# Optimization experiments

Hardware: AMD Instinct MI355X
Metric: run time of the kernel (lower is better)

## Reference

```python
import jax, jax.numpy as jnp
import numpy as np

NUM_HEADS = 12


def _build_mask(N, unseen_size, dtype):
    # Columns for the last `unseen_size` tokens are masked (-inf) for every
    # query row EXCEPT the diagonal entries in that block (each unseen token
    # may attend to itself). Matches the original Python-loop construction.
    idx = jnp.arange(N)
    col_unseen = idx[None, :] >= (N - unseen_size)
    off_diag = idx[:, None] != idx[None, :]
    return jnp.where(col_unseen & off_diag, -jnp.inf, jnp.asarray(0.0, dtype))


def reference(x, w_qkv, w_proj, b_proj, unseen_size):
    B, N, C = x.shape
    H = NUM_HEADS
    d = C // H
    scale = d ** -0.5
    # qkv: (B,N,3C) -> (3,B,H,N,d)
    qkv = (x @ w_qkv.T).reshape(B, N, 3, H, d).transpose(2, 0, 3, 1, 4)
    q, k, v = qkv[0], qkv[1], qkv[2]
    attn = jnp.einsum('bhqd,bhkd->bhqk', q, k) * scale
    attn = attn + _build_mask(N, unseen_size, attn.dtype)  # broadcast (N,N)
    attn = jax.nn.softmax(attn, axis=-1)
    out = jnp.einsum('bhqk,bhkd->bhqd', attn, v)
    out = out.transpose(0, 2, 1, 3).reshape(B, N, C)
    return out @ w_proj.T + b_proj


def setup_inputs() -> dict:
    key = jax.random.key(0)
    k1, k2, k3 = jax.random.split(key, 3)
    B, N, C = 2, 2048, 768
    x = jax.random.normal(k1, (B, N, C), dtype=jnp.float32)
    w_qkv = jax.random.normal(k2, (3 * C, C), dtype=jnp.float32) * (C ** -0.5)
    w_proj = jax.random.normal(k3, (C, C), dtype=jnp.float32) * (C ** -0.5)
    b_proj = jnp.zeros((C,), dtype=jnp.float32)
    return {"x": x, "w_qkv": w_qkv, "w_proj": w_proj, "b_proj": b_proj,
            "unseen_size": 512}
```

## Files before the change

kernel.cpp:

```cpp
#include <hip/hip_runtime.h>
#include <math.h>

#define NH 12
#define DH 64
#define NSEQ 2048
#define NB 2
#define CDIM 768
#define NVIS 1536

typedef _Float16 half8 __attribute__((ext_vector_type(8)));
typedef _Float16 half4 __attribute__((ext_vector_type(4)));
typedef float floatx4 __attribute__((ext_vector_type(4)));

static constexpr size_t SZ_X    = (size_t)NB*NSEQ*CDIM;
static constexpr size_t SZ_WQKV = (size_t)3*CDIM*CDIM;
static constexpr size_t SZ_WP   = (size_t)CDIM*CDIM;
static constexpr size_t SZ_HEAD = (size_t)NB*NH*NSEQ*DH;

#define GLOAD_LDS16(gp, lp) \
  __builtin_amdgcn_global_load_lds((const __attribute__((address_space(1))) void*)(gp), \
                                   (__attribute__((address_space(3))) void*)(lp), 16, 0, 0)

__global__ __launch_bounds__(256) void convert_kernel(
    const float* __restrict__ x, const float* __restrict__ wqkv, const float* __restrict__ wp,
    _Float16* __restrict__ xb, _Float16* __restrict__ wqkvb, _Float16* __restrict__ wpb)
{
  size_t idx = ((size_t)blockIdx.x*256 + threadIdx.x)*4;
  const float* src; _Float16* dst; size_t off;
  if (idx < SZ_X)                        { src = x;    dst = xb;    off = idx; }
  else if (idx < SZ_X+SZ_WQKV)           { src = wqkv; dst = wqkvb; off = idx - SZ_X; }
  else if (idx < SZ_X+SZ_WQKV+SZ_WP)     { src = wp;   dst = wpb;   off = idx - SZ_X - SZ_WQKV; }
  else return;
  float4 v = *reinterpret_cast<const float4*>(src + off);
  _Float16 o[4] = {(_Float16)v.x,(_Float16)v.y,(_Float16)v.z,(_Float16)v.w};
  *reinterpret_cast<uint2*>(dst + off) = *reinterpret_cast<uint2*>(o);
}

template<int MODE, int BN>
__global__ __launch_bounds__(256) void gemm_bt(
    const _Float16* __restrict__ A, const _Float16* __restrict__ Bt,
    const float* __restrict__ bias,
    _Float16* __restrict__ qb, _Float16* __restrict__ kb, _Float16* __restrict__ vb,
    float* __restrict__ outp)
{
  constexpr int K = CDIM;
  constexpr int BM = 128, BK = 32;
  constexpr int MI = (BN == 128) ? 4 : 2;
  constexpr int NI = 4;
  __shared__ _Float16 As[BM*BK];
  __shared__ _Float16 Bs[BN*BK];
  const int tid = threadIdx.x;
  const int lane = tid & 63, wid = tid >> 6;
  const int l15 = lane & 15, quad = lane >> 4;
  const int wm = (BN == 128) ? (wid >> 1)*64 : wid*32;
  const int wn = (BN == 128) ? (wid & 1)*64 : 0;
  const int tileN = blockIdx.x*BN, tileM = blockIdx.y*BM;
  const int lrow = lane >> 2, lchunk = lane & 3;
  const int gcol = ((lchunk ^ (lrow >> 1)) & 3)*8;
  const _Float16* gA0 = A  + (size_t)(tileM + wid*32      + lrow)*K + gcol;
  const _Float16* gA1 = A  + (size_t)(tileM + wid*32 + 16 + lrow)*K + gcol;
  const _Float16* gB0 = Bt + (size_t)(tileN + ((BN==128) ? wid*32 : wid*16) + lrow)*K + gcol;
  const _Float16* gB1 = Bt + (size_t)(tileN + wid*32 + 16 + lrow)*K + gcol;
  _Float16* lA0 = As + (wid*32)*BK;
  _Float16* lA1 = As + (wid*32 + 16)*BK;
  _Float16* lB0 = Bs + ((BN==128) ? wid*32 : wid*16)*BK;
  _Float16* lB1 = Bs + (wid*32 + 16)*BK;
  const int cp = ((quad ^ (l15 >> 1)) & 3)*8;
  floatx4 acc[MI][NI] = {};
  for (int k0 = 0; k0 < K; k0 += BK) {
    __syncthreads();
    GLOAD_LDS16(gA0 + k0, lA0);
    GLOAD_LDS16(gA1 + k0, lA1);
    GLOAD_LDS16(gB0 + k0, lB0);
    if (BN == 128) GLOAD_LDS16(gB1 + k0, lB1);
    __syncthreads();
    half8 af[MI], bfr[NI];
    #pragma unroll
    for (int mi = 0; mi < MI; mi++)
      af[mi] = *reinterpret_cast<const half8*>(&As[(wm + mi*16 + l15)*BK + cp]);
    #pragma unroll
    for (int ni = 0; ni < NI; ni++)
      bfr[ni] = *reinterpret_cast<const half8*>(&Bs[(wn + ni*16 + l15)*BK + cp]);
    #pragma unroll
    for (int mi = 0; mi < MI; mi++)
      #pragma unroll
      for (int ni = 0; ni < NI; ni++)
        acc[mi][ni] = __builtin_amdgcn_mfma_f32_16x16x32_f16(af[mi], bfr[ni], acc[mi][ni], 0,0,0);
  }
  #pragma unroll
  for (int mi = 0; mi < MI; mi++)
    #pragma unroll
    for (int ni = 0; ni < NI; ni++) {
      int n = tileN + wn + ni*16 + l15;
      int m0 = tileM + wm + mi*16 + quad*4;
      if (MODE == 0) {
        int part = n / CDIM, rem = n - part*CDIM;
        int h = rem >> 6, dd = rem & 63;
        int b = m0 >> 11, i0 = m0 & 2047;
        if (part == 2) {
          half4 pk = {(_Float16)acc[mi][ni][0], (_Float16)acc[mi][ni][1],
                      (_Float16)acc[mi][ni][2], (_Float16)acc[mi][ni][3]};
          *reinterpret_cast<half4*>(&vb[(((size_t)b*NH + h)*DH + dd)*NSEQ + i0]) = pk;
        } else {
          _Float16* dst = part ? kb : qb;
          float sc = part ? 1.0f : 0.125f*1.44269504f;
          #pragma unroll
          for (int r = 0; r < 4; r++)
            dst[(((size_t)b*NH + h)*NSEQ + i0 + r)*DH + dd] = (_Float16)(acc[mi][ni][r]*sc);
        }
      } else {
        #pragma unroll
        for (int r = 0; r < 4; r++)
          outp[(size_t)(m0 + r)*CDIM + n] = acc[mi][ni][r] + bias[n];
      }
    }
}

__global__ __launch_bounds__(256, 3) void fa_kernel(
    const _Float16* __restrict__ qg, const _Float16* __restrict__ kg,
    const _Float16* __restrict__ vtg, _Float16* __restrict__ og)
{
  constexpr int LDP = 136;
  __shared__ _Float16 Ps[64*LDP];
  __shared__ float Ls[4*64];
  const int blk = blockIdx.x;
  const int idx = blk >> 3;
  const int bh = (blk & 7)*3 + (idx % 3);
  const int qbase = (idx / 3) * 64;
  const int tid = threadIdx.x;
  const int lane = tid & 63, w = tid >> 6;
  const int l15 = lane & 15, quad = lane >> 4;
  const _Float16* qp  = qg  + (size_t)bh*NSEQ*DH;
  const _Float16* kbp = kg  + (size_t)bh*NSEQ*DH;
  const _Float16* vbp = vtg + (size_t)bh*DH*NSEQ;
  half8 qf[4][2];
  #pragma unroll
  for (int g = 0; g < 4; g++)
    #pragma unroll
    for (int c = 0; c < 2; c++)
      qf[g][c] = *reinterpret_cast<const half8*>(qp + (size_t)(qbase + g*16 + l15)*DH + c*32 + quad*8);
  const _Float16* kRow = kbp + (size_t)(w*16 + l15)*DH + quad*8;
  const _Float16* vRow = vbp + (size_t)(w*16 + l15)*NSEQ + quad*8;
  half8 kc[2][2], vc[2][2];
  #pragma unroll
  for (int s = 0; s < 2; s++)
    #pragma unroll
    for (int c = 0; c < 2; c++) {
      kc[s][c] = *reinterpret_cast<const half8*>(kRow + (size_t)(s*64)*DH + c*32);
      vc[s][c] = *reinterpret_cast<const half8*>(vRow + s*64 + c*32);
    }
  floatx4 o[4] = {};
  float lsum[4] = {0.f, 0.f, 0.f, 0.f};
  for (int t = 0; t < 12; t++) {
    const int tn = (t + 1 < 12) ? t + 1 : 0;
    half8 kn[2][2], vn[2][2];
    #pragma unroll
    for (int s = 0; s < 2; s++)
      #pragma unroll
      for (int c = 0; c < 2; c++) {
        kn[s][c] = *reinterpret_cast<const half8*>(kRow + (size_t)(tn*128 + s*64)*DH + c*32);
        vn[s][c] = *reinterpret_cast<const half8*>(vRow + tn*128 + s*64 + c*32);
      }
    half4 pk[2][4];
    #pragma unroll
    for (int s = 0; s < 2; s++) {
      floatx4 st[4] = {};
      #pragma unroll
      for (int g = 0; g < 4; g++) {
        st[g] = __builtin_amdgcn_mfma_f32_16x16x32_f16(kc[s][0], qf[g][0], st[g], 0,0,0);
        st[g] = __builtin_amdgcn_mfma_f32_16x16x32_f16(kc[s][1], qf[g][1], st[g], 0,0,0);
      }
      #pragma unroll
      for (int g = 0; g < 4; g++) {
        float e0 = __builtin_exp2f(st[g][0]), e1 = __builtin_exp2f(st[g][1]);
        float e2 = __builtin_exp2f(st[g][2]), e3 = __builtin_exp2f(st[g][3]);
        lsum[g] += (e0+e1)+(e2+e3);
        pk[s][g] = half4{(_Float16)e0,(_Float16)e1,(_Float16)e2,(_Float16)e3};
      }
    }
    __syncthreads();
    #pragma unroll
    for (int s = 0; s < 2; s++)
      #pragma unroll
      for (int g = 0; g < 4; g++)
        *reinterpret_cast<half4*>(&Ps[(g*16+l15)*LDP + s*64 + w*16 + quad*4]) = pk[s][g];
    __syncthreads();
    #pragma unroll
    for (int g = 0; g < 4; g++) {
      #pragma unroll
      for (int s = 0; s < 2; s++)
        #pragma unroll
        for (int c = 0; c < 2; c++) {
          half8 pb = *reinterpret_cast<const half8*>(&Ps[(g*16+l15)*LDP + s*64 + c*32 + quad*8]);
          o[g] = __builtin_amdgcn_mfma_f32_16x16x32_f16(vc[s][c], pb, o[g], 0,0,0);
        }
    }
    #pragma unroll
    for (int s = 0; s < 2; s++)
      #pragma unroll
      for (int c = 0; c < 2; c++) { kc[s][c] = kn[s][c]; vc[s][c] = vn[s][c]; }
  }
  #pragma unroll
  for (int g = 0; g < 4; g++) {
    lsum[g] += __shfl_xor(lsum[g], 16);
    lsum[g] += __shfl_xor(lsum[g], 32);
  }
  if (lane < 16) {
    #pragma unroll
    for (int g = 0; g < 4; g++) Ls[w*64 + g*16 + lane] = lsum[g];
  }
  __syncthreads();
  float den[4];
  #pragma unroll
  for (int g = 0; g < 4; g++)
    den[g] = Ls[g*16+l15] + Ls[64+g*16+l15] + Ls[128+g*16+l15] + Ls[192+g*16+l15];
  if (qbase >= NVIS) {
    #pragma unroll
    for (int g = 0; g < 4; g++) {
      half8 kd0 = *reinterpret_cast<const half8*>(kbp + (size_t)(qbase + g*16 + l15)*DH + quad*8);
      half8 kd1 = *reinterpret_cast<const half8*>(kbp + (size_t)(qbase + g*16 + l15)*DH + 32 + quad*8);
      float pd = 0.f;
      #pragma unroll
      for (int j = 0; j < 8; j++)
        pd += (float)qf[g][0][j]*(float)kd0[j] + (float)qf[g][1][j]*(float)kd1[j];
      pd += __shfl_xor(pd, 16);
      pd += __shfl_xor(pd, 32);
      float e = __builtin_exp2f(pd);
      den[g] += e;
      #pragma unroll
      for (int r = 0; r < 4; r++)
        o[g][r] += e * (float)vbp[(size_t)(w*16+quad*4+r)*NSEQ + qbase + g*16 + l15];
    }
  }
  const int b = bh / NH, h = bh - b*NH;
  #pragma unroll
  for (int g = 0; g < 4; g++) {
    float inv = 1.0f / den[g];
    half4 pk = {(_Float16)(o[g][0]*inv), (_Float16)(o[g][1]*inv),
                (_Float16)(o[g][2]*inv), (_Float16)(o[g][3]*inv)};
    size_t oaddr = ((size_t)b*NSEQ + qbase + g*16 + l15)*CDIM + h*DH + w*16 + quad*4;
    *reinterpret_cast<half4*>(&og[oaddr]) = pk;
  }
}

extern "C" void kernel_launch(void* const* d_in, const int* in_sizes, int n_in,
                              void* d_out, int out_size, void* d_ws, size_t ws_size,
                              hipStream_t stream) {
  (void)in_sizes; (void)n_in; (void)out_size; (void)ws_size;
  const float* x     = (const float*)d_in[0];
  const float* wqkv  = (const float*)d_in[1];
  const float* wproj = (const float*)d_in[2];
  const float* bproj = (const float*)d_in[3];

  _Float16* xb    = (_Float16*)d_ws;
  _Float16* wqkvb = xb + SZ_X;
  _Float16* wpb   = wqkvb + SZ_WQKV;
  _Float16* qb    = wpb + SZ_WP;
  _Float16* kb    = qb + SZ_HEAD;
  _Float16* vb    = kb + SZ_HEAD;
  _Float16* ob    = vb + SZ_HEAD;
  float* outp = (float*)d_out;

  size_t total = SZ_X + SZ_WQKV + SZ_WP;
  int cblocks = (int)((total/4 + 255)/256);
  convert_kernel<<<cblocks, 256, 0, stream>>>(x, wqkv, wproj, xb, wqkvb, wpb);
  gemm_bt<0,128><<<dim3(3*CDIM/128, NB*NSEQ/128), 256, 0, stream>>>(xb, wqkvb, nullptr, qb, kb, vb, nullptr);
  fa_kernel<<<NB*NH*(NSEQ/64), 256, 0, stream>>>(qb, kb, vb, ob);
  gemm_bt<1,64><<<dim3(CDIM/64, NB*NSEQ/128), 256, 0, stream>>>(ob, wpb, bproj, nullptr, nullptr, nullptr, outp);
}
```

Before: 166.0 us.

## Restructure attention kernel: LDS double-buffered K/V, register-shuffled P, 2 waves

The attention kernel moves from 4 waves that each load their own K/V slices from global into registers and exchange P through LDS with two barriers per step, to 2 waves that each own 32 query rows. K and V tiles of 64 keys are now staged into swizzled, double-buffered LDS with async global-to-LDS loads. P is repacked in registers with cross-lane shuffles and packed fp16 conversion instead of going through shared memory. The aim is to remove the P round-trip through LDS and the duplicated K/V fetches, at the cost of more shuffles, fewer waves per block, and a lower occupancy hint.

```diff
diff --git a/kernel.cpp b/kernel.cpp
--- a/kernel.cpp
+++ b/kernel.cpp
@@ -10,6 +10,7 @@
 
 typedef _Float16 half8 __attribute__((ext_vector_type(8)));
 typedef _Float16 half4 __attribute__((ext_vector_type(4)));
+typedef __fp16 fp16x2 __attribute__((ext_vector_type(2)));
 typedef float floatx4 __attribute__((ext_vector_type(4)));
 
 static constexpr size_t SZ_X    = (size_t)NB*NSEQ*CDIM;
@@ -20,6 +21,12 @@
 #define GLOAD_LDS16(gp, lp) \
   __builtin_amdgcn_global_load_lds((const __attribute__((address_space(1))) void*)(gp), \
                                    (__attribute__((address_space(3))) void*)(lp), 16, 0, 0)
+
+static __device__ __forceinline__ int pack_e2(float a, float b) {
+  union { fp16x2 h; int i; } u;
+  u.h = __builtin_amdgcn_cvt_pkrtz(a, b);
+  return u.i;
+}
 
 __global__ __launch_bounds__(256) void convert_kernel(
     const float* __restrict__ x, const float* __restrict__ wqkv, const float* __restrict__ wp,
@@ -116,13 +123,12 @@
     }
 }
 
-__global__ __launch_bounds__(256, 3) void fa_kernel(
+__global__ __launch_bounds__(128, 2) void fa_kernel(
     const _Float16* __restrict__ qg, const _Float16* __restrict__ kg,
     const _Float16* __restrict__ vtg, _Float16* __restrict__ og)
 {
-  constexpr int LDP = 136;
-  __shared__ _Float16 Ps[64*LDP];
-  __shared__ float Ls[4*64];
+  __shared__ _Float16 Ks[2][64*64];
+  __shared__ _Float16 Vs[2][64*64];
   const int blk = blockIdx.x;
   const int idx = blk >> 3;
   const int bh = (blk & 7)*3 + (idx % 3);
@@ -133,92 +139,95 @@
   const _Float16* qp  = qg  + (size_t)bh*NSEQ*DH;
   const _Float16* kbp = kg  + (size_t)bh*NSEQ*DH;
   const _Float16* vbp = vtg + (size_t)bh*DH*NSEQ;
-  half8 qf[4][2];
-  #pragma unroll
-  for (int g = 0; g < 4; g++)
+  half8 qf[2][2];
+  #pragma unroll
+  for (int g = 0; g < 2; g++)
     #pragma unroll
     for (int c = 0; c < 2; c++)
-      qf[g][c] = *reinterpret_cast<const half8*>(qp + (size_t)(qbase + g*16 + l15)*DH + c*32 + quad*8);
-  const _Float16* kRow = kbp + (size_t)(w*16 + l15)*DH + quad*8;
-  const _Float16* vRow = vbp + (size_t)(w*16 + l15)*NSEQ + quad*8;
-  half8 kc[2][2], vc[2][2];
-  #pragma unroll
-  for (int s = 0; s < 2; s++)
-    #pragma unroll
-    for (int c = 0; c < 2; c++) {
-      kc[s][c] = *reinterpret_cast<const half8*>(kRow + (size_t)(s*64)*DH + c*32);
-      vc[s][c] = *reinterpret_cast<const half8*>(vRow + s*64 + c*32);
-    }
-  floatx4 o[4] = {};
-  float lsum[4] = {0.f, 0.f, 0.f, 0.f};
-  for (int t = 0; t < 12; t++) {
-    const int tn = (t + 1 < 12) ? t + 1 : 0;
-    half8 kn[2][2], vn[2][2];
-    #pragma unroll
-    for (int s = 0; s < 2; s++)
+      qf[g][c] = *reinterpret_cast<const half8*>(
+          qp + (size_t)(qbase + w*32 + g*16 + l15)*DH + c*32 + quad*8);
+  const int strow = w*32 + (lane >> 3);
+  const int sgch  = ((lane & 7) ^ (lane >> 3)) * 8;
+  const int rdoff0 = l15*64 + (((0*4 + quad) ^ (l15 & 7))*8);
+  const int rdoff1 = l15*64 + (((1*4 + quad) ^ (l15 & 7))*8);
+  const int bidx0 = ((quad & 1)*2)*16 + l15;
+  const int bidx1 = bidx0 + 16;
+  const bool hiq = (quad >> 1) != 0;
+
+  floatx4 o[2][4] = {};
+  float lsum[2] = {0.f, 0.f};
+
+  #pragma unroll
+  for (int u = 0; u < 4; u++) {
+    GLOAD_LDS16(kbp + (size_t)(strow + u*8)*DH + sgch,        &Ks[0][(w*32 + u*8)*64]);
+    GLOAD_LDS16(vbp + (size_t)(strow + u*8)*NSEQ + 0 + sgch,  &Vs[0][(w*32 + u*8)*64]);
+  }
+  for (int t = 0; t < 24; t++) {
+    const int buf = t & 1;
+    __syncthreads();
+    if (t < 23) {
+      const int kvn = (t + 1)*64;
+      #pragma unroll
+      for (int u = 0; u < 4; u++) {
+        GLOAD_LDS16(kbp + (size_t)(kvn + strow + u*8)*DH + sgch,   &Ks[buf^1][(w*32 + u*8)*64]);
+        GLOAD_LDS16(vbp + (size_t)(strow + u*8)*NSEQ + kvn + sgch, &Vs[buf^1][(w*32 + u*8)*64]);
+      }
+    }
+    half8 kf[4][2], vf[4][2];
+    #pragma unroll
+    for (int f = 0; f < 4; f++) {
+      kf[f][0] = *reinterpret_cast<const half8*>(&Ks[buf][f*1024 + rdoff0]);
+      kf[f][1] = *reinterpret_cast<const half8*>(&Ks[buf][f*1024 + rdoff1]);
+      vf[f][0] = *reinterpret_cast<const half8*>(&Vs[buf][f*1024 + rdoff0]);
+      vf[f][1] = *reinterpret_cast<const half8*>(&Vs[buf][f*1024 + rdoff1]);
+    }
+    int srcdw[2][4][2];
+    #pragma unroll
+    for (int g = 0; g < 2; g++)
+      #pragma unroll
+      for (int f = 0; f < 4; f++) {
+        floatx4 st = {};
+        st = __builtin_amdgcn_mfma_f32_16x16x32_f16(kf[f][0], qf[g][0], st, 0,0,0);
+        st = __builtin_amdgcn_mfma_f32_16x16x32_f16(kf[f][1], qf[g][1], st, 0,0,0);
+        float e0 = __builtin_exp2f(st[0]), e1 = __builtin_exp2f(st[1]);
+        float e2 = __builtin_exp2f(st[2]), e3 = __builtin_exp2f(st[3]);
+        lsum[g] += (e0 + e1) + (e2 + e3);
+        srcdw[g][f][0] = pack_e2(e0, e1);
+        srcdw[g][f][1] = pack_e2(e2, e3);
+      }
+    #pragma unroll
+    for (int g = 0; g < 2; g++) {
       #pragma unroll
       for (int c = 0; c < 2; c++) {
-        kn[s][c] = *reinterpret_cast<const half8*>(kRow + (size_t)(tn*128 + s*64)*DH + c*32);
-        vn[s][c] = *reinterpret_cast<const half8*>(vRow + tn*128 + s*64 + c*32);
-      }
-    half4 pk[2][4];
-    #pragma unroll
-    for (int s = 0; s < 2; s++) {
-      floatx4 st[4] = {};
-      #pragma unroll
-      for (int g = 0; g < 4; g++) {
-        st[g] = __builtin_amdgcn_mfma_f32_16x16x32_f16(kc[s][0], qf[g][0], st[g], 0,0,0);
-        st[g] = __builtin_amdgcn_mfma_f32_16x16x32_f16(kc[s][1], qf[g][1], st[g], 0,0,0);
-      }
-      #pragma unroll
-      for (int g = 0; g < 4; g++) {
-        float e0 = __builtin_exp2f(st[g][0]), e1 = __builtin_exp2f(st[g][1]);
-        float e2 = __builtin_exp2f(st[g][2]), e3 = __builtin_exp2f(st[g][3]);
-        lsum[g] += (e0+e1)+(e2+e3);
-        pk[s][g] = half4{(_Float16)e0,(_Float16)e1,(_Float16)e2,(_Float16)e3};
-      }
-    }
-    __syncthreads();
-    #pragma unroll
-    for (int s = 0; s < 2; s++)
-      #pragma unroll
-      for (int g = 0; g < 4; g++)
-        *reinterpret_cast<half4*>(&Ps[(g*16+l15)*LDP + s*64 + w*16 + quad*4]) = pk[s][g];
-    __syncthreads();
-    #pragma unroll
-    for (int g = 0; g < 4; g++) {
-      #pragma unroll
-      for (int s = 0; s < 2; s++)
+        union { int i[4]; half8 v; } pbu;
         #pragma unroll
-        for (int c = 0; c < 2; c++) {
-          half8 pb = *reinterpret_cast<const half8*>(&Ps[(g*16+l15)*LDP + s*64 + c*32 + quad*8]);
-          o[g] = __builtin_amdgcn_mfma_f32_16x16x32_f16(vc[s][c], pb, o[g], 0,0,0);
+        for (int p = 0; p < 4; p++) {
+          const int ix = (p >> 1) ? bidx1 : bidx0;
+          int tA = __shfl(srcdw[g][2*c][p & 1], ix);
+          int tB = __shfl(srcdw[g][2*c + 1][p & 1], ix);
+          pbu.i[p] = hiq ? tB : tA;
         }
-    }
-    #pragma unroll
-    for (int s = 0; s < 2; s++)
-      #pragma unroll
-      for (int c = 0; c < 2; c++) { kc[s][c] = kn[s][c]; vc[s][c] = vn[s][c]; }
-  }
-  #pragma unroll
-  for (int g = 0; g < 4; g++) {
-    lsum[g] += __shfl_xor(lsum[g], 16);
-    lsum[g] += __shfl_xor(lsum[g], 32);
-  }
-  if (lane < 16) {
-    #pragma unroll
-    for (int g = 0; g < 4; g++) Ls[w*64 + g*16 + lane] = lsum[g];
-  }
-  __syncthreads();
-  float den[4];
-  #pragma unroll
-  for (int g = 0; g < 4; g++)
-    den[g] = Ls[g*16+l15] + Ls[64+g*16+l15] + Ls[128+g*16+l15] + Ls[192+g*16+l15];
+        o[g][0] = __builtin_amdgcn_mfma_f32_16x16x32_f16(vf[0][c], pbu.v, o[g][0], 0,0,0);
+        o[g][1] = __builtin_amdgcn_mfma_f32_16x16x32_f16(vf[1][c], pbu.v, o[g][1], 0,0,0);
+        o[g][2] = __builtin_amdgcn_mfma_f32_16x16x32_f16(vf[2][c], pbu.v, o[g][2], 0,0,0);
+        o[g][3] = __builtin_amdgcn_mfma_f32_16x16x32_f16(vf[3][c], pbu.v, o[g][3], 0,0,0);
+      }
+    }
+  }
+  float den[2];
+  #pragma unroll
+  for (int g = 0; g < 2; g++) {
+    float s = lsum[g];
+    s += __shfl_xor(s, 16);
+    s += __shfl_xor(s, 32);
+    den[g] = s;
+  }
   if (qbase >= NVIS) {
     #pragma unroll
-    for (int g = 0; g < 4; g++) {
-      half8 kd0 = *reinterpret_cast<const half8*>(kbp + (size_t)(qbase + g*16 + l15)*DH + quad*8);
-      half8 kd1 = *reinterpret_cast<const half8*>(kbp + (size_t)(qbase + g*16 + l15)*DH + 32 + quad*8);
+    for (int g = 0; g < 2; g++) {
+      const int q_abs = qbase + w*32 + g*16 + l15;
+      half8 kd0 = *reinterpret_cast<const half8*>(kbp + (size_t)q_abs*DH + quad*8);
+      half8 kd1 = *reinterpret_cast<const half8*>(kbp + (size_t)q_abs*DH + 32 + quad*8);
       float pd = 0.f;
       #pragma unroll
       for (int j = 0; j < 8; j++)
@@ -228,18 +237,24 @@
       float e = __builtin_exp2f(pd);
       den[g] += e;
       #pragma unroll
-      for (int r = 0; r < 4; r++)
-        o[g][r] += e * (float)vbp[(size_t)(w*16+quad*4+r)*NSEQ + qbase + g*16 + l15];
+      for (int df = 0; df < 4; df++)
+        #pragma unroll
+        for (int r = 0; r < 4; r++)
+          o[g][df][r] += e * (float)vbp[(size_t)(df*16 + quad*4 + r)*NSEQ + q_abs];
     }
   }
   const int b = bh / NH, h = bh - b*NH;
   #pragma unroll
-  for (int g = 0; g < 4; g++) {
-    float inv = 1.0f / den[g];
-    half4 pk = {(_Float16)(o[g][0]*inv), (_Float16)(o[g][1]*inv),
-                (_Float16)(o[g][2]*inv), (_Float16)(o[g][3]*inv)};
-    size_t oaddr = ((size_t)b*NSEQ + qbase + g*16 + l15)*CDIM + h*DH + w*16 + quad*4;
-    *reinterpret_cast<half4*>(&og[oaddr]) = pk;
+  for (int g = 0; g < 2; g++) {
+    const float inv = 1.0f / den[g];
+    const int q_abs = qbase + w*32 + g*16 + l15;
+    size_t obase = ((size_t)b*NSEQ + q_abs)*CDIM + h*DH + quad*4;
+    #pragma unroll
+    for (int df = 0; df < 4; df++) {
+      half4 pk = {(_Float16)(o[g][df][0]*inv), (_Float16)(o[g][df][1]*inv),
+                  (_Float16)(o[g][df][2]*inv), (_Float16)(o[g][df][3]*inv)};
+      *reinterpret_cast<half4*>(&og[obase + df*16]) = pk;
+    }
   }
 }
 
@@ -265,6 +280,6 @@
   int cblocks = (int)((total/4 + 255)/256);
   convert_kernel<<<cblocks, 256, 0, stream>>>(x, wqkv, wproj, xb, wqkvb, wpb);
   gemm_bt<0,128><<<dim3(3*CDIM/128, NB*NSEQ/128), 256, 0, stream>>>(xb, wqkvb, nullptr, qb, kb, vb, nullptr);
-  fa_kernel<<<NB*NH*(NSEQ/64), 256, 0, stream>>>(qb, kb, vb, ob);
+  fa_kernel<<<NB*NH*(NSEQ/64), 128, 0, stream>>>(qb, kb, vb, ob);
   gemm_bt<1,64><<<dim3(CDIM/64, NB*NSEQ/128), 256, 0, stream>>>(ob, wpb, bproj, nullptr, nullptr, nullptr, outp);
 }
```

Measured after the change: 175.5 us. 1.06x slower.

## Split attention KV range across two blocks and add combine kernel

Applied to the files above, without the earlier changes.

The attention kernel now splits the 1536 visible keys into two halves handled by separate blocks, doubling the grid and halving the per-iteration tile. It writes unnormalized fp32 partial outputs and denominators to workspace. A new combine kernel sums the partials, adds the diagonal unseen term and normalizes. The aim is better occupancy and more parallelism (768 to 1536 blocks, launch bounds 6). The cost is an extra launch and fp32 partial traffic through global memory.

```diff
diff --git a/kernel.cpp b/kernel.cpp
--- a/kernel.cpp
+++ b/kernel.cpp
@@ -16,6 +16,8 @@
 static constexpr size_t SZ_WQKV = (size_t)3*CDIM*CDIM;
 static constexpr size_t SZ_WP   = (size_t)CDIM*CDIM;
 static constexpr size_t SZ_HEAD = (size_t)NB*NH*NSEQ*DH;
+static constexpr size_t SZ_OPART = (size_t)2*24*32*64*64;
+static constexpr size_t SZ_DEN   = (size_t)2*24*32*64;
 
 #define GLOAD_LDS16(gp, lp) \
   __builtin_amdgcn_global_load_lds((const __attribute__((address_space(1))) void*)(gp), \
@@ -116,17 +118,22 @@
     }
 }
 
-__global__ __launch_bounds__(256, 3) void fa_kernel(
+__global__ __launch_bounds__(256, 6) void fa_kernel(
     const _Float16* __restrict__ qg, const _Float16* __restrict__ kg,
-    const _Float16* __restrict__ vtg, _Float16* __restrict__ og)
+    const _Float16* __restrict__ vtg, float* __restrict__ opart,
+    float* __restrict__ denp)
 {
-  constexpr int LDP = 136;
+  constexpr int LDP = 72;
   __shared__ _Float16 Ps[64*LDP];
   __shared__ float Ls[4*64];
   const int blk = blockIdx.x;
   const int idx = blk >> 3;
   const int bh = (blk & 7)*3 + (idx % 3);
-  const int qbase = (idx / 3) * 64;
+  const int rest = idx / 3;
+  const int qtile = rest >> 1;
+  const int sb = rest & 1;
+  const int qbase = qtile * 64;
+  const int kvoff = sb * 768;
   const int tid = threadIdx.x;
   const int lane = tid & 63, w = tid >> 6;
   const int l15 = lane & 15, quad = lane >> 4;
@@ -139,66 +146,47 @@
     #pragma unroll
     for (int c = 0; c < 2; c++)
       qf[g][c] = *reinterpret_cast<const half8*>(qp + (size_t)(qbase + g*16 + l15)*DH + c*32 + quad*8);
-  const _Float16* kRow = kbp + (size_t)(w*16 + l15)*DH + quad*8;
-  const _Float16* vRow = vbp + (size_t)(w*16 + l15)*NSEQ + quad*8;
-  half8 kc[2][2], vc[2][2];
-  #pragma unroll
-  for (int s = 0; s < 2; s++)
-    #pragma unroll
-    for (int c = 0; c < 2; c++) {
-      kc[s][c] = *reinterpret_cast<const half8*>(kRow + (size_t)(s*64)*DH + c*32);
-      vc[s][c] = *reinterpret_cast<const half8*>(vRow + s*64 + c*32);
-    }
+  const _Float16* kRow = kbp + (size_t)(kvoff + w*16 + l15)*DH + quad*8;
+  const _Float16* vRow = vbp + (size_t)(w*16 + l15)*NSEQ + kvoff + quad*8;
+  half8 kc0 = *reinterpret_cast<const half8*>(kRow);
+  half8 kc1 = *reinterpret_cast<const half8*>(kRow + 32);
+  half8 vc0 = *reinterpret_cast<const half8*>(vRow);
+  half8 vc1 = *reinterpret_cast<const half8*>(vRow + 32);
   floatx4 o[4] = {};
   float lsum[4] = {0.f, 0.f, 0.f, 0.f};
   for (int t = 0; t < 12; t++) {
     const int tn = (t + 1 < 12) ? t + 1 : 0;
-    half8 kn[2][2], vn[2][2];
-    #pragma unroll
-    for (int s = 0; s < 2; s++)
-      #pragma unroll
-      for (int c = 0; c < 2; c++) {
-        kn[s][c] = *reinterpret_cast<const half8*>(kRow + (size_t)(tn*128 + s*64)*DH + c*32);
-        vn[s][c] = *reinterpret_cast<const half8*>(vRow + tn*128 + s*64 + c*32);
-      }
-    half4 pk[2][4];
-    #pragma unroll
-    for (int s = 0; s < 2; s++) {
-      floatx4 st[4] = {};
-      #pragma unroll
-      for (int g = 0; g < 4; g++) {
-        st[g] = __builtin_amdgcn_mfma_f32_16x16x32_f16(kc[s][0], qf[g][0], st[g], 0,0,0);
-        st[g] = __builtin_amdgcn_mfma_f32_16x16x32_f16(kc[s][1], qf[g][1], st[g], 0,0,0);
-      }
-      #pragma unroll
-      for (int g = 0; g < 4; g++) {
-        float e0 = __builtin_exp2f(st[g][0]), e1 = __builtin_exp2f(st[g][1]);
-        float e2 = __builtin_exp2f(st[g][2]), e3 = __builtin_exp2f(st[g][3]);
-        lsum[g] += (e0+e1)+(e2+e3);
-        pk[s][g] = half4{(_Float16)e0,(_Float16)e1,(_Float16)e2,(_Float16)e3};
-      }
+    half8 kn0 = *reinterpret_cast<const half8*>(kRow + (size_t)tn*64*DH);
+    half8 kn1 = *reinterpret_cast<const half8*>(kRow + (size_t)tn*64*DH + 32);
+    half8 vn0 = *reinterpret_cast<const half8*>(vRow + tn*64);
+    half8 vn1 = *reinterpret_cast<const half8*>(vRow + tn*64 + 32);
+    floatx4 st[4] = {};
+    #pragma unroll
+    for (int g = 0; g < 4; g++) {
+      st[g] = __builtin_amdgcn_mfma_f32_16x16x32_f16(kc0, qf[g][0], st[g], 0,0,0);
+      st[g] = __builtin_amdgcn_mfma_f32_16x16x32_f16(kc1, qf[g][1], st[g], 0,0,0);
+    }
+    half4 pk[4];
+    #pragma unroll
+    for (int g = 0; g < 4; g++) {
+      float e0 = __builtin_exp2f(st[g][0]), e1 = __builtin_exp2f(st[g][1]);
+      float e2 = __builtin_exp2f(st[g][2]), e3 = __builtin_exp2f(st[g][3]);
+      lsum[g] += (e0+e1)+(e2+e3);
+      pk[g] = half4{(_Float16)e0,(_Float16)e1,(_Float16)e2,(_Float16)e3};
     }
     __syncthreads();
     #pragma unroll
-    for (int s = 0; s < 2; s++)
-      #pragma unroll
-      for (int g = 0; g < 4; g++)
-        *reinterpret_cast<half4*>(&Ps[(g*16+l15)*LDP + s*64 + w*16 + quad*4]) = pk[s][g];
+    for (int g = 0; g < 4; g++)
+      *reinterpret_cast<half4*>(&Ps[(g*16+l15)*LDP + w*16 + quad*4]) = pk[g];
     __syncthreads();
     #pragma unroll
     for (int g = 0; g < 4; g++) {
-      #pragma unroll
-      for (int s = 0; s < 2; s++)
-        #pragma unroll
-        for (int c = 0; c < 2; c++) {
-          half8 pb = *reinterpret_cast<const half8*>(&Ps[(g*16+l15)*LDP + s*64 + c*32 + quad*8]);
-          o[g] = __builtin_amdgcn_mfma_f32_16x16x32_f16(vc[s][c], pb, o[g], 0,0,0);
-        }
+      half8 pb0 = *reinterpret_cast<const half8*>(&Ps[(g*16+l15)*LDP + quad*8]);
+      half8 pb1 = *reinterpret_cast<const half8*>(&Ps[(g*16+l15)*LDP + 32 + quad*8]);
+      o[g] = __builtin_amdgcn_mfma_f32_16x16x32_f16(vc0, pb0, o[g], 0,0,0);
+      o[g] = __builtin_amdgcn_mfma_f32_16x16x32_f16(vc1, pb1, o[g], 0,0,0);
     }
-    #pragma unroll
-    for (int s = 0; s < 2; s++)
-      #pragma unroll
-      for (int c = 0; c < 2; c++) { kc[s][c] = kn[s][c]; vc[s][c] = vn[s][c]; }
+    kc0 = kn0; kc1 = kn1; vc0 = vn0; vc1 = vn1;
   }
   #pragma unroll
   for (int g = 0; g < 4; g++) {
@@ -210,37 +198,78 @@
     for (int g = 0; g < 4; g++) Ls[w*64 + g*16 + lane] = lsum[g];
   }
   __syncthreads();
-  float den[4];
+  float* op = opart + (((size_t)sb*24 + bh)*32 + qtile)*4096;
   #pragma unroll
   for (int g = 0; g < 4; g++)
-    den[g] = Ls[g*16+l15] + Ls[64+g*16+l15] + Ls[128+g*16+l15] + Ls[192+g*16+l15];
+    #pragma unroll
+    for (int r = 0; r < 4; r++)
+      op[(w*16 + quad*4 + r)*64 + g*16 + l15] = o[g][r];
+  if (w == 0) {
+    float dsum = Ls[lane] + Ls[64+lane] + Ls[128+lane] + Ls[192+lane];
+    denp[(((size_t)sb*24 + bh)*32 + qtile)*64 + lane] = dsum;
+  }
+}
+
+__global__ __launch_bounds__(256) void combine_kernel(
+    const float* __restrict__ opart, const float* __restrict__ denp,
+    const _Float16* __restrict__ qg, const _Float16* __restrict__ kg,
+    const _Float16* __restrict__ vtg, _Float16* __restrict__ og)
+{
+  __shared__ float Ot[64*65];
+  __shared__ float Dn[64];
+  const int bh = blockIdx.x >> 5;
+  const int qtile = blockIdx.x & 31;
+  const int qbase = qtile * 64;
+  const int t = threadIdx.x;
+  const float* opA = opart + ((size_t)bh*32 + qtile)*4096;
+  const float* opB = opart + ((size_t)(24 + bh)*32 + qtile)*4096;
+  if (t < 64)
+    Dn[t] = denp[((size_t)bh*32 + qtile)*64 + t]
+          + denp[((size_t)(24 + bh)*32 + qtile)*64 + t];
+  #pragma unroll
+  for (int i = 0; i < 16; i++) {
+    int idx = i*256 + t;
+    int d = idx >> 6, q = idx & 63;
+    Ot[d*65 + q] = opA[idx] + opB[idx];
+  }
+  __syncthreads();
+  const int q = t >> 2, ds = (t & 3)*16;
+  const int q_abs = qbase + q;
+  float ov[16];
+  #pragma unroll
+  for (int j = 0; j < 16; j++) ov[j] = Ot[(ds + j)*65 + q];
+  float den = Dn[q];
   if (qbase >= NVIS) {
-    #pragma unroll
-    for (int g = 0; g < 4; g++) {
-      half8 kd0 = *reinterpret_cast<const half8*>(kbp + (size_t)(qbase + g*16 + l15)*DH + quad*8);
-      half8 kd1 = *reinterpret_cast<const half8*>(kbp + (size_t)(qbase + g*16 + l15)*DH + 32 + quad*8);
-      float pd = 0.f;
-      #pragma unroll
-      for (int j = 0; j < 8; j++)
-        pd += (float)qf[g][0][j]*(float)kd0[j] + (float)qf[g][1][j]*(float)kd1[j];
-      pd += __shfl_xor(pd, 16);
-      pd += __shfl_xor(pd, 32);
-      float e = __builtin_exp2f(pd);
-      den[g] += e;
-      #pragma unroll
-      for (int r = 0; r < 4; r++)
-        o[g][r] += e * (float)vbp[(size_t)(w*16+quad*4+r)*NSEQ + qbase + g*16 + l15];
-    }
-  }
+    const _Float16* qrow = qg + ((size_t)bh*NSEQ + q_abs)*DH + ds;
+    const _Float16* krow = kg + ((size_t)bh*NSEQ + q_abs)*DH + ds;
+    half8 qa = *reinterpret_cast<const half8*>(qrow);
+    half8 qb2 = *reinterpret_cast<const half8*>(qrow + 8);
+    half8 ka = *reinterpret_cast<const half8*>(krow);
+    half8 kb2 = *reinterpret_cast<const half8*>(krow + 8);
+    float pd = 0.f;
+    #pragma unroll
+    for (int j = 0; j < 8; j++)
+      pd += (float)qa[j]*(float)ka[j] + (float)qb2[j]*(float)kb2[j];
+    pd += __shfl_xor(pd, 1);
+    pd += __shfl_xor(pd, 2);
+    float e = __builtin_exp2f(pd);
+    den += e;
+    const _Float16* vcol = vtg + (size_t)bh*DH*NSEQ + q_abs;
+    #pragma unroll
+    for (int j = 0; j < 16; j++)
+      ov[j] += e * (float)vcol[(size_t)(ds + j)*NSEQ];
+  }
+  const float inv = 1.0f / den;
   const int b = bh / NH, h = bh - b*NH;
-  #pragma unroll
-  for (int g = 0; g < 4; g++) {
-    float inv = 1.0f / den[g];
-    half4 pk = {(_Float16)(o[g][0]*inv), (_Float16)(o[g][1]*inv),
-                (_Float16)(o[g][2]*inv), (_Float16)(o[g][3]*inv)};
-    size_t oaddr = ((size_t)b*NSEQ + qbase + g*16 + l15)*CDIM + h*DH + w*16 + quad*4;
-    *reinterpret_cast<half4*>(&og[oaddr]) = pk;
-  }
+  size_t base = ((size_t)b*NSEQ + q_abs)*CDIM + h*DH + ds;
+  half8 h0, h1;
+  #pragma unroll
+  for (int j = 0; j < 8; j++) {
+    h0[j] = (_Float16)(ov[j]*inv);
+    h1[j] = (_Float16)(ov[8 + j]*inv);
+  }
+  *reinterpret_cast<half8*>(&og[base])     = h0;
+  *reinterpret_cast<half8*>(&og[base + 8]) = h1;
 }
 
 extern "C" void kernel_launch(void* const* d_in, const int* in_sizes, int n_in,
@@ -259,12 +288,15 @@
   _Float16* kb    = qb + SZ_HEAD;
   _Float16* vb    = kb + SZ_HEAD;
   _Float16* ob    = vb + SZ_HEAD;
+  float* opart = (float*)(ob + SZ_HEAD);
+  float* denp  = opart + SZ_OPART;
   float* outp = (float*)d_out;
 
   size_t total = SZ_X + SZ_WQKV + SZ_WP;
   int cblocks = (int)((total/4 + 255)/256);
   convert_kernel<<<cblocks, 256, 0, stream>>>(x, wqkv, wproj, xb, wqkvb, wpb);
   gemm_bt<0,128><<<dim3(3*CDIM/128, NB*NSEQ/128), 256, 0, stream>>>(xb, wqkvb, nullptr, qb, kb, vb, nullptr);
-  fa_kernel<<<NB*NH*(NSEQ/64), 256, 0, stream>>>(qb, kb, vb, ob);
+  fa_kernel<<<NB*NH*(NSEQ/64)*2, 256, 0, stream>>>(qb, kb, vb, opart, denp);
+  combine_kernel<<<NB*NH*(NSEQ/64), 256, 0, stream>>>(opart, denp, qb, kb, vb, ob);
   gemm_bt<1,64><<<dim3(CDIM/64, NB*NSEQ/128), 256, 0, stream>>>(ob, wpb, bproj, nullptr, nullptr, nullptr, outp);
 }
```

Result: slower. 279.7 us (+68.5%).

## Software-pipeline attention loop with double-buffered P tile and one barrier per step

Applied to the files above, without the earlier changes.

Restructures the flash-attention main loop to process 64-key tiles over 24 steps instead of 128-key tiles over 12. The score/exp of tile t+1 is written into one of two LDS P buffers while the PV MFMAs consume the other, which cuts the barriers per step from two to one and overlaps softmax with the PV product. It adds a prologue and epilogue. Smaller tiles mean more loop iterations and barriers in total, but fewer live registers.

```diff
diff --git a/kernel.cpp b/kernel.cpp
--- a/kernel.cpp
+++ b/kernel.cpp
@@ -120,8 +120,8 @@
     const _Float16* __restrict__ qg, const _Float16* __restrict__ kg,
     const _Float16* __restrict__ vtg, _Float16* __restrict__ og)
 {
-  constexpr int LDP = 136;
-  __shared__ _Float16 Ps[64*LDP];
+  constexpr int LDP = 72;
+  __shared__ _Float16 Ps[2][64*LDP];
   __shared__ float Ls[4*64];
   const int blk = blockIdx.x;
   const int idx = blk >> 3;
@@ -141,64 +141,72 @@
       qf[g][c] = *reinterpret_cast<const half8*>(qp + (size_t)(qbase + g*16 + l15)*DH + c*32 + quad*8);
   const _Float16* kRow = kbp + (size_t)(w*16 + l15)*DH + quad*8;
   const _Float16* vRow = vbp + (size_t)(w*16 + l15)*NSEQ + quad*8;
-  half8 kc[2][2], vc[2][2];
-  #pragma unroll
-  for (int s = 0; s < 2; s++)
-    #pragma unroll
-    for (int c = 0; c < 2; c++) {
-      kc[s][c] = *reinterpret_cast<const half8*>(kRow + (size_t)(s*64)*DH + c*32);
-      vc[s][c] = *reinterpret_cast<const half8*>(vRow + s*64 + c*32);
-    }
   floatx4 o[4] = {};
   float lsum[4] = {0.f, 0.f, 0.f, 0.f};
-  for (int t = 0; t < 12; t++) {
-    const int tn = (t + 1 < 12) ? t + 1 : 0;
-    half8 kn[2][2], vn[2][2];
-    #pragma unroll
-    for (int s = 0; s < 2; s++)
-      #pragma unroll
-      for (int c = 0; c < 2; c++) {
-        kn[s][c] = *reinterpret_cast<const half8*>(kRow + (size_t)(tn*128 + s*64)*DH + c*32);
-        vn[s][c] = *reinterpret_cast<const half8*>(vRow + tn*128 + s*64 + c*32);
-      }
-    half4 pk[2][4];
-    #pragma unroll
-    for (int s = 0; s < 2; s++) {
-      floatx4 st[4] = {};
-      #pragma unroll
-      for (int g = 0; g < 4; g++) {
-        st[g] = __builtin_amdgcn_mfma_f32_16x16x32_f16(kc[s][0], qf[g][0], st[g], 0,0,0);
-        st[g] = __builtin_amdgcn_mfma_f32_16x16x32_f16(kc[s][1], qf[g][1], st[g], 0,0,0);
-      }
-      #pragma unroll
-      for (int g = 0; g < 4; g++) {
-        float e0 = __builtin_exp2f(st[g][0]), e1 = __builtin_exp2f(st[g][1]);
-        float e2 = __builtin_exp2f(st[g][2]), e3 = __builtin_exp2f(st[g][3]);
-        lsum[g] += (e0+e1)+(e2+e3);
-        pk[s][g] = half4{(_Float16)e0,(_Float16)e1,(_Float16)e2,(_Float16)e3};
-      }
+
+  half8 kcur0 = *reinterpret_cast<const half8*>(kRow);
+  half8 kcur1 = *reinterpret_cast<const half8*>(kRow + 32);
+  {
+    floatx4 st[4] = {};
+    #pragma unroll
+    for (int g = 0; g < 4; g++) {
+      st[g] = __builtin_amdgcn_mfma_f32_16x16x32_f16(kcur0, qf[g][0], st[g], 0,0,0);
+      st[g] = __builtin_amdgcn_mfma_f32_16x16x32_f16(kcur1, qf[g][1], st[g], 0,0,0);
+    }
+    #pragma unroll
+    for (int g = 0; g < 4; g++) {
+      float e0 = __builtin_exp2f(st[g][0]), e1 = __builtin_exp2f(st[g][1]);
+      float e2 = __builtin_exp2f(st[g][2]), e3 = __builtin_exp2f(st[g][3]);
+      lsum[g] += (e0+e1)+(e2+e3);
+      half4 pk = {(_Float16)e0,(_Float16)e1,(_Float16)e2,(_Float16)e3};
+      *reinterpret_cast<half4*>(&Ps[0][(g*16+l15)*LDP + w*16 + quad*4]) = pk;
+    }
+  }
+  half8 vcur0 = *reinterpret_cast<const half8*>(vRow);
+  half8 vcur1 = *reinterpret_cast<const half8*>(vRow + 32);
+  kcur0 = *reinterpret_cast<const half8*>(kRow + (size_t)64*DH);
+  kcur1 = *reinterpret_cast<const half8*>(kRow + (size_t)64*DH + 32);
+
+  for (int t = 0; t < 23; t++) {
+    const int tk = (t + 2 < 24) ? t + 2 : 0;
+    half8 kn0 = *reinterpret_cast<const half8*>(kRow + (size_t)tk*64*DH);
+    half8 kn1 = *reinterpret_cast<const half8*>(kRow + (size_t)tk*64*DH + 32);
+    half8 vn0 = *reinterpret_cast<const half8*>(vRow + (t+1)*64);
+    half8 vn1 = *reinterpret_cast<const half8*>(vRow + (t+1)*64 + 32);
+    floatx4 st[4] = {};
+    #pragma unroll
+    for (int g = 0; g < 4; g++) {
+      st[g] = __builtin_amdgcn_mfma_f32_16x16x32_f16(kcur0, qf[g][0], st[g], 0,0,0);
+      st[g] = __builtin_amdgcn_mfma_f32_16x16x32_f16(kcur1, qf[g][1], st[g], 0,0,0);
+    }
+    half4 pk[4];
+    #pragma unroll
+    for (int g = 0; g < 4; g++) {
+      float e0 = __builtin_exp2f(st[g][0]), e1 = __builtin_exp2f(st[g][1]);
+      float e2 = __builtin_exp2f(st[g][2]), e3 = __builtin_exp2f(st[g][3]);
+      lsum[g] += (e0+e1)+(e2+e3);
+      pk[g] = half4{(_Float16)e0,(_Float16)e1,(_Float16)e2,(_Float16)e3};
     }
     __syncthreads();
     #pragma unroll
-    for (int s = 0; s < 2; s++)
-      #pragma unroll
-      for (int g = 0; g < 4; g++)
-        *reinterpret_cast<half4*>(&Ps[(g*16+l15)*LDP + s*64 + w*16 + quad*4]) = pk[s][g];
-    __syncthreads();
-    #pragma unroll
-    for (int g = 0; g < 4; g++) {
-      #pragma unroll
-      for (int s = 0; s < 2; s++)
-        #pragma unroll
-        for (int c = 0; c < 2; c++) {
-          half8 pb = *reinterpret_cast<const half8*>(&Ps[(g*16+l15)*LDP + s*64 + c*32 + quad*8]);
-          o[g] = __builtin_amdgcn_mfma_f32_16x16x32_f16(vc[s][c], pb, o[g], 0,0,0);
-        }
-    }
-    #pragma unroll
-    for (int s = 0; s < 2; s++)
-      #pragma unroll
-      for (int c = 0; c < 2; c++) { kc[s][c] = kn[s][c]; vc[s][c] = vn[s][c]; }
+    for (int g = 0; g < 4; g++)
+      *reinterpret_cast<half4*>(&Ps[(t+1)&1][(g*16+l15)*LDP + w*16 + quad*4]) = pk[g];
+    #pragma unroll
+    for (int g = 0; g < 4; g++) {
+      half8 pb0 = *reinterpret_cast<const half8*>(&Ps[t&1][(g*16+l15)*LDP + quad*8]);
+      half8 pb1 = *reinterpret_cast<const half8*>(&Ps[t&1][(g*16+l15)*LDP + 32 + quad*8]);
+      o[g] = __builtin_amdgcn_mfma_f32_16x16x32_f16(vcur0, pb0, o[g], 0,0,0);
+      o[g] = __builtin_amdgcn_mfma_f32_16x16x32_f16(vcur1, pb1, o[g], 0,0,0);
+    }
+    kcur0 = kn0; kcur1 = kn1; vcur0 = vn0; vcur1 = vn1;
+  }
+  __syncthreads();
+  #pragma unroll
+  for (int g = 0; g < 4; g++) {
+    half8 pb0 = *reinterpret_cast<const half8*>(&Ps[1][(g*16+l15)*LDP + quad*8]);
+    half8 pb1 = *reinterpret_cast<const half8*>(&Ps[1][(g*16+l15)*LDP + 32 + quad*8]);
+    o[g] = __builtin_amdgcn_mfma_f32_16x16x32_f16(vcur0, pb0, o[g], 0,0,0);
+    o[g] = __builtin_amdgcn_mfma_f32_16x16x32_f16(vcur1, pb1, o[g], 0,0,0);
   }
   #pragma unroll
   for (int g = 0; g < 4; g++) {
```

Result: faster. 160.5 us (-3.3%).
